# Kernel tuning notes

Measured on AMD Instinct MI355X. Metric: run time of the kernel, lower is better.

Reference implementation:

```python
import jax, jax.numpy as jnp
import numpy as np

B, L = 1, 2048
D_MODEL, N_LAYER, D_INNER = 768, 2, 1536
D_STATE, DT_RANK, D_CONV, OUT_DIM = 16, 48, 4, 128


def setup_inputs() -> dict:
    key = jax.random.key(0)
    ks = jax.random.split(key, 10)
    s = 0.02
    p = {}
    p["x"] = jax.random.normal(ks[0], (B, L, D_MODEL), jnp.float32)
    # stacked per-layer parameters, leading dim = N_LAYER
    p["in_proj_w"] = jax.random.normal(ks[1], (N_LAYER, 2 * D_INNER, D_MODEL), jnp.float32) * s
    p["conv_w"] = jax.random.normal(ks[2], (N_LAYER, D_INNER, D_CONV), jnp.float32) * s
    p["conv_b"] = jnp.zeros((N_LAYER, D_INNER), jnp.float32)
    p["x_proj_w"] = jax.random.normal(ks[3], (N_LAYER, DT_RANK + 2 * D_STATE, D_INNER), jnp.float32) * s
    p["dt_proj_w"] = jax.random.normal(ks[4], (N_LAYER, D_INNER, DT_RANK), jnp.float32) * s
    p["dt_proj_b"] = jax.random.normal(ks[5], (N_LAYER, D_INNER), jnp.float32) * s
    A = jnp.tile(jnp.arange(1, D_STATE + 1, dtype=jnp.float32)[None, :], (D_INNER, 1))
    p["A_log"] = jnp.tile(jnp.log(A)[None], (N_LAYER, 1, 1))
    p["D"] = jnp.ones((N_LAYER, D_INNER), jnp.float32)
    p["out_proj_w"] = jax.random.normal(ks[6], (N_LAYER, D_MODEL, D_INNER), jnp.float32) * s
    p["norm_w"] = jnp.ones((N_LAYER, D_MODEL), jnp.float32)
    p["norm_f_w"] = jnp.ones((D_MODEL,), jnp.float32)
    p["head_w"] = jax.random.normal(ks[7], (OUT_DIM, D_MODEL), jnp.float32) * s
    return p


def rmsnorm(x, w, eps=1e-5):
    return x * jax.lax.rsqrt(jnp.mean(x * x, -1, keepdims=True) + eps) * w


def selective_scan(u, delta, A, Bm, Cm, Dv):
    # u, delta: (b,l,d); A: (d,n); Bm, Cm: (b,l,n); Dv: (d,)
    dA = jnp.exp(jnp.einsum('bld,dn->bldn', delta, A))       # discretized A
    dBu = jnp.einsum('bld,bln->bldn', delta * u, Bm)          # discretized B*u

    def step(s, inp):
        dA_t, dBu_t, C_t = inp                               # (b,d,n),(b,d,n),(b,n)
        s = dA_t * s + dBu_t
        y = jnp.einsum('bdn,bn->bd', s, C_t)
        return s, y

    s0 = jnp.zeros((u.shape[0], u.shape[2], A.shape[1]), u.dtype)
    _, ys = jax.lax.scan(step, s0, (dA.transpose(1, 0, 2, 3), dBu.transpose(1, 0, 2, 3), Cm.transpose(1, 0, 2)))
    y = ys.transpose(1, 0, 2)                                # (b,l,d)
    return y + u * Dv


def mamba_block(x, w):
    xr = jnp.einsum('bld,ed->ble', x, w['in_proj_w'])        # (b,l,2*d_inner)
    xin, res = jnp.split(xr, 2, axis=-1)
    # causal depthwise conv1d
    xc = jax.lax.conv_general_dilated(
        xin.transpose(0, 2, 1), w['conv_w'][:, None, :],
        window_strides=(1,), padding=[(D_CONV - 1, 0)],
        dimension_numbers=('NCH', 'OIH', 'NCH'),
        feature_group_count=D_INNER)
    xc = (xc + w['conv_b'][None, :, None]).transpose(0, 2, 1)
    xc = jax.nn.silu(xc)
    # SSM
    A = -jnp.exp(w['A_log'])                                 # (d_inner, d_state)
    proj = jnp.einsum('bld,ed->ble', xc, w['x_proj_w'])
    delta, Bm, Cm = jnp.split(proj, [DT_RANK, DT_RANK + D_STATE], axis=-1)
    delta = jax.nn.softplus(jnp.einsum('blr,dr->bld', delta, w['dt_proj_w']) + w['dt_proj_b'])
    y = selective_scan(xc, delta, A, Bm, Cm, w['D'])
    y = y * jax.nn.silu(res)
    return jnp.einsum('bld,ed->ble', y, w['out_proj_w'])


def reference(x, in_proj_w, conv_w, conv_b, x_proj_w, dt_proj_w, dt_proj_b,
              A_log, D, out_proj_w, norm_w, norm_f_w, head_w):
    stacked = dict(in_proj_w=in_proj_w, conv_w=conv_w, conv_b=conv_b,
                   x_proj_w=x_proj_w, dt_proj_w=dt_proj_w, dt_proj_b=dt_proj_b,
                   A_log=A_log, D=D, out_proj_w=out_proj_w)
    for i in range(N_LAYER):
        w = {k: v[i] for k, v in stacked.items()}
        x = x + mamba_block(rmsnorm(x, norm_w[i]), w)        # pre-norm residual block
    x = rmsnorm(x, norm_f_w)
    return jnp.einsum('bld,od->blo', x, head_w)              # lm_head (no bias)
```

## Files before the change

kernel.cpp:

```cpp
#include <hip/hip_runtime.h>
#include <hip/hip_bf16.h>
#include <stdint.h>

#define LSEQ 2048
#define DM 768
#define DI 1536
#define NCH 128
#define CHK 16

typedef __bf16 bf16;
typedef short short8 __attribute__((ext_vector_type(8)));
typedef float floatx4 __attribute__((ext_vector_type(4)));
typedef bf16 bf16x8 __attribute__((ext_vector_type(8)));

__device__ inline float silu_f(float x){ return x / (1.f + __expf(-x)); }

__device__ __forceinline__ void g2l16(const bf16* g, bf16* l){
  __builtin_amdgcn_global_load_lds(
      (const __attribute__((address_space(1))) void*)g,
      (__attribute__((address_space(3))) void*)l, 16, 0, 0);
}

__device__ inline int bf16_flag(const void* dvv){
  return (*(const unsigned*)dvv == 0x3F803F80u) ? 1 : 0;
}

__device__ inline float ldin(const void* p, long i, int f){
  return f ? (float)((const bf16*)p)[i] : ((const float*)p)[i];
}

__device__ __forceinline__ void ld8(const void* src, long i, int f, float* o){
  if(f){
    bf16x8 v = *(const bf16x8*)((const bf16*)src + i);
    #pragma unroll
    for(int k = 0; k < 8; k++) o[k] = (float)v[k];
  } else {
    float4 a = ((const float4*)src)[i >> 2];
    float4 b = ((const float4*)src)[(i >> 2) + 1];
    o[0]=a.x; o[1]=a.y; o[2]=a.z; o[3]=a.w; o[4]=b.x; o[5]=b.y; o[6]=b.z; o[7]=b.w;
  }
}
__device__ __forceinline__ void st8_bf(bf16* dst, long i, const float* o){
  bf16x8 v;
  #pragma unroll
  for(int k = 0; k < 8; k++) v[k] = (bf16)o[k];
  *(bf16x8*)(dst + i) = v;
}
__device__ __forceinline__ void st8_f32(float* dst, long i, const float* o){
  ((float4*)dst)[i >> 2]       = make_float4(o[0], o[1], o[2], o[3]);
  ((float4*)dst)[(i >> 2) + 1] = make_float4(o[4], o[5], o[6], o[7]);
}

#define NB_INW  2304
#define NB_OUTW 1152
#define NB_HW   48
#define NB_X    768
#define NB_ALOG 24
#define NB_XPW  192
#define NB_DTW  96
#define NB_SM   12
#define NB_TOT  (NB_INW+NB_OUTW+NB_HW+NB_X+NB_ALOG+NB_XPW+NB_DTW+NB_SM)

__global__ __launch_bounds__(256) void k_canon(const void* x_, const void* inw_,
    const void* cw_, const void* cb_, const void* xpw_, const void* dtw_,
    const void* dtb_, const void* dvv_, const void* alog_, const void* outw_,
    const void* nw_, const void* nfw_, const void* hw_,
    float* x0, bf16* inw, float* cw, float* cb, bf16* xpw, bf16* dtw, float* dtb,
    float* alog, float* dv, bf16* outw, float* nw, float* nfw, bf16* hw){
  int f = bf16_flag(dvv_);
  int b = blockIdx.x;
  int t = threadIdx.x;
  float o[8];
  if(b < NB_INW + NB_OUTW + NB_HW){
    const void* src; bf16* dst; long off;
    if(b < NB_INW){ src = inw_; dst = inw; off = (long)b*2048; }
    else if(b < NB_INW + NB_OUTW){ src = outw_; dst = outw; off = (long)(b - NB_INW)*2048; }
    else { src = hw_; dst = hw; off = (long)(b - NB_INW - NB_OUTW)*2048; }
    long i = off + t*8;
    if(f){ *(bf16x8*)(dst + i) = *(const bf16x8*)((const bf16*)src + i); }
    else { ld8(src, i, 0, o); st8_bf(dst, i, o); }
    return;
  }
  b -= NB_INW + NB_OUTW + NB_HW;
  if(b < NB_X + NB_ALOG){
    const void* src; float* dst; long off;
    if(b < NB_X){ src = x_; dst = x0; off = (long)b*2048; }
    else { src = alog_; dst = alog; off = (long)(b - NB_X)*2048; }
    long i = off + t*8;
    ld8(src, i, f, o);
    st8_f32(dst, i, o);
    return;
  }
  b -= NB_X + NB_ALOG;
  if(b < NB_XPW){
    long j = (long)b*2048 + t*8;
    int layer = (int)(j / (128*DI));
    int rem = (int)(j % (128*DI));
    int r = rem / DI, c = rem % DI;
    if(r < 80){
      ld8(xpw_, ((long)layer*80 + r)*DI + c, f, o);
    } else {
      for(int k = 0; k < 8; k++) o[k] = 0.f;
    }
    st8_bf(xpw, j, o);
    return;
  }
  b -= NB_XPW;
  if(b < NB_DTW){
    long j = (long)b*2048 + t*8;
    int layer = (int)(j / (DI*64));
    int rem = (int)(j % (DI*64));
    int r = rem / 64, c = rem % 64;
    if(c < 48){
      ld8(dtw_, ((long)layer*DI + r)*48 + c, f, o);
    } else {
      for(int k = 0; k < 8; k++) o[k] = 0.f;
    }
    st8_bf(dtw, j, o);
    return;
  }
  b -= NB_DTW;
  for(int idx = b*256 + t; idx < 23808; idx += NB_SM*256){
    int j = idx;
    if(j < 12288){ cw[j] = ldin(cw_, j, f); continue; } j -= 12288;
    if(j < 3072){ cb[j] = ldin(cb_, j, f); continue; } j -= 3072;
    if(j < 3072){ dtb[j] = ldin(dtb_, j, f); continue; } j -= 3072;
    if(j < 3072){ dv[j] = ldin(dvv_, j, f); continue; } j -= 3072;
    if(j < 1536){ nw[j] = ldin(nw_, j, f); continue; } j -= 1536;
    nfw[j] = ldin(nfw_, j, f);
  }
}

__global__ __launch_bounds__(256) void k_rmsnorm(const float* __restrict__ x,
    const float* __restrict__ w, bf16* __restrict__ out){
  int row = blockIdx.x;
  const float* xr = x + row*DM;
  int t = threadIdx.x;
  float v0 = xr[t], v1 = xr[t+256], v2 = xr[t+512];
  float ss = v0*v0 + v1*v1 + v2*v2;
  #pragma unroll
  for(int o = 32; o; o >>= 1) ss += __shfl_down(ss, o, 64);
  __shared__ float red[4];
  int lane = t & 63, wid = t >> 6;
  if(lane == 0) red[wid] = ss;
  __syncthreads();
  ss = red[0] + red[1] + red[2] + red[3];
  float rs = rsqrtf(ss / DM + 1e-5f);
  out[row*DM + t]       = (bf16)(v0 * rs * w[t]);
  out[row*DM + t + 256] = (bf16)(v1 * rs * w[t+256]);
  out[row*DM + t + 512] = (bf16)(v2 * rs * w[t+512]);
}

template<int SPLITK, int MODE>
__global__ __launch_bounds__(256) void k_gemm(
    const bf16* __restrict__ A, const bf16* __restrict__ B, void* Cv,
    int K, int ldc, const float* __restrict__ aux){
  __shared__ bf16 sA[64*32];
  __shared__ bf16 sB[128*32];
  int bm0 = blockIdx.y*64, bn0 = blockIdx.x*128;
  int tid = threadIdx.x;
  int lane = tid & 63, wid = tid >> 6;
  int wn = wid*32;
  int quad = lane >> 4, lr = lane & 15;
  const int klen = K / SPLITK;
  const int kbeg = (SPLITK > 1) ? blockIdx.z * klen : 0;
  const bf16* Ag = A + (size_t)(bm0 + (tid>>2))*K + kbeg + (tid&3)*8;
  const bf16* Bg = B + (size_t)(bn0 + (tid>>2))*K + kbeg + (tid&3)*8;
  floatx4 acc[4][2] = {};
  for(int k0 = 0; k0 < klen; k0 += 32){
    __syncthreads();
    g2l16(Ag, sA + tid*8);
    g2l16(Bg, sB + tid*8);
    g2l16(Bg + 64*K, sB + 2048 + tid*8);
    __syncthreads();
    short8 af[4], bf_[2];
    #pragma unroll
    for(int i = 0; i < 4; i++)
      af[i]  = *(const short8*)(sA + (i*16 + lr)*32 + quad*8);
    #pragma unroll
    for(int j = 0; j < 2; j++)
      bf_[j] = *(const short8*)(sB + (wn + j*16 + lr)*32 + quad*8);
    #pragma unroll
    for(int i = 0; i < 4; i++)
      #pragma unroll
      for(int j = 0; j < 2; j++)
        acc[i][j] = __builtin_amdgcn_mfma_f32_16x16x32_bf16(af[i], bf_[j], acc[i][j], 0, 0, 0);
    Ag += 32; Bg += 32;
  }
  float* Cf = (float*)Cv + ((MODE == 5) ? (size_t)blockIdx.z * LSEQ * ldc : 0);
  bf16* Cb = (bf16*)Cv;
  #pragma unroll
  for(int i = 0; i < 4; i++){
    #pragma unroll
    for(int j = 0; j < 2; j++){
      #pragma unroll
      for(int r = 0; r < 4; r++){
        int grow = bm0 + i*16 + quad*4 + r;
        int gcol = bn0 + wn + j*16 + lr;
        float v = acc[i][j][r];
        if(MODE == 0){
          Cb[(size_t)grow*ldc + gcol] = (bf16)v;
        } else if(MODE == 1){
          v += aux[gcol];
          v = fmaxf(v, 0.f) + log1pf(__expf(-fabsf(v)));
          Cb[(size_t)grow*ldc + gcol] = (bf16)v;
        } else {
          Cf[(size_t)grow*ldc + gcol] = v;
        }
      }
    }
  }
  (void)aux;
}

__global__ __launch_bounds__(256) void k_epi_xproj(const float* __restrict__ part,
    float* __restrict__ proj, bf16* __restrict__ dtin){
  int idx = blockIdx.x*256 + threadIdx.x;
  float s = 0.f;
  #pragma unroll
  for(int z = 0; z < 8; z++) s += part[(size_t)z*LSEQ*128 + idx];
  int row = idx >> 7, col = idx & 127;
  if(col < 80) proj[row*80 + col] = s;
  if(col < 64) dtin[row*64 + col] = (col < 48) ? (bf16)s : (bf16)0.f;
}

__global__ __launch_bounds__(256) void k_epi_out_norm(const float* __restrict__ part,
    const float* __restrict__ resid, const float* __restrict__ w,
    float* __restrict__ xws, bf16* __restrict__ xn){
  int row = blockIdx.x;
  int t = threadIdx.x;
  float v[3]; float ss = 0.f;
  #pragma unroll
  for(int k = 0; k < 3; k++){
    long i = (long)row*DM + t + k*256;
    float s = part[i] + part[(long)LSEQ*DM + i] + resid[i];
    xws[i] = s; v[k] = s; ss += s*s;
  }
  #pragma unroll
  for(int o = 32; o; o >>= 1) ss += __shfl_down(ss, o, 64);
  __shared__ float red[4];
  if((t & 63) == 0) red[t >> 6] = ss;
  __syncthreads();
  ss = red[0] + red[1] + red[2] + red[3];
  float rs = rsqrtf(ss / DM + 1e-5f);
  #pragma unroll
  for(int k = 0; k < 3; k++){
    int col = t + k*256;
    xn[(long)row*DM + col] = (bf16)(v[k] * rs * w[col]);
  }
}

__global__ __launch_bounds__(256) void k_epi_head(const float* __restrict__ part,
    const void* dvv, void* out){
  int idx = blockIdx.x*256 + threadIdx.x;
  const int N = LSEQ*128;
  float s = part[idx] + part[N+idx] + part[2*N+idx] + part[3*N+idx];
  if(bf16_flag(dvv)) ((bf16*)out)[idx] = (bf16)s;
  else               ((float*)out)[idx] = s;
}

__global__ __launch_bounds__(256) void k_conv(const bf16* __restrict__ xr,
    const float* __restrict__ cw, const float* __restrict__ cb,
    bf16* __restrict__ xcb){
  int d = blockIdx.x*256 + threadIdx.x;
  int l0 = blockIdx.y*16;
  float w0 = cw[d*4+0], w1 = cw[d*4+1], w2 = cw[d*4+2], w3 = cw[d*4+3];
  float bias = cb[d];
  float xm3 = (l0 >= 3) ? (float)xr[(l0-3)*(2*DI) + d] : 0.f;
  float xm2 = (l0 >= 2) ? (float)xr[(l0-2)*(2*DI) + d] : 0.f;
  float xm1 = (l0 >= 1) ? (float)xr[(l0-1)*(2*DI) + d] : 0.f;
  #pragma unroll
  for(int tl = 0; tl < 16; tl++){
    int l = l0 + tl;
    float xc = (float)xr[l*(2*DI) + d];
    float acc = bias + xm3*w0 + xm2*w1 + xm1*w2 + xc*w3;
    xcb[l*DI + d] = (bf16)silu_f(acc);
    xm3 = xm2; xm2 = xm1; xm1 = xc;
  }
}

__global__ __launch_bounds__(256) void k_scan1(
    const bf16* __restrict__ delta, const bf16* __restrict__ u,
    const float* __restrict__ proj, const float* __restrict__ alog,
    float* __restrict__ Aprod, float* __restrict__ Bsum){
  int d = blockIdx.y*256 + threadIdx.x;
  int c = blockIdx.x;
  __shared__ float Bl[CHK*16];
  {
    int t = threadIdx.x >> 4, n = threadIdx.x & 15;
    Bl[threadIdx.x] = proj[(c*CHK + t)*80 + 48 + n];
  }
  __syncthreads();
  const float L2E = 1.44269504f;
  float An2[16], ap[16], s[16];
  #pragma unroll
  for(int n = 0; n < 16; n++){ An2[n] = -__expf(alog[d*16+n]) * L2E; ap[n] = 1.f; s[n] = 0.f; }
  int t0 = c*CHK;
  float dt = (float)delta[t0*DI + d];
  float uu = (float)u[t0*DI + d];
  #pragma unroll
  for(int tl = 0; tl < CHK; tl++){
    float dtn = 0.f, un = 0.f;
    if(tl + 1 < CHK){
      dtn = (float)delta[(t0+tl+1)*DI + d];
      un = (float)u[(t0+tl+1)*DI + d];
    }
    float du = dt * uu;
    #pragma unroll
    for(int n = 0; n < 16; n++){
      float e = exp2f(dt * An2[n]);
      s[n] = e*s[n] + du*Bl[tl*16+n];
      ap[n] *= e;
    }
    dt = dtn; uu = un;
  }
  int base = (c*DI + d)*16;
  #pragma unroll
  for(int n = 0; n < 16; n++){ Aprod[base+n] = ap[n]; Bsum[base+n] = s[n]; }
}

__global__ __launch_bounds__(256) void k_scan2(float* __restrict__ Aprod,
    const float* __restrict__ Bsum){
  int idx = blockIdx.x*256 + threadIdx.x;
  float s = 0.f;
  for(int c = 0; c < NCH; c++){
    int o = c*DI*16 + idx;
    float a = Aprod[o], b = Bsum[o];
    Aprod[o] = s;
    s = a*s + b;
  }
}

__global__ __launch_bounds__(256) void k_scan3(
    const bf16* __restrict__ delta, const bf16* __restrict__ u,
    const float* __restrict__ proj, const float* __restrict__ alog,
    const float* __restrict__ dvp, const float* __restrict__ Sinit,
    const bf16* __restrict__ xr, bf16* __restrict__ ybar){
  int d = blockIdx.y*256 + threadIdx.x;
  int c = blockIdx.x;
  __shared__ float Bl[CHK*16], Cl[CHK*16];
  {
    int t = threadIdx.x >> 4, n = threadIdx.x & 15;
    Bl[threadIdx.x] = proj[(c*CHK + t)*80 + 48 + n];
    Cl[threadIdx.x] = proj[(c*CHK + t)*80 + 64 + n];
  }
  __syncthreads();
  const float L2E = 1.44269504f;
  float An2[16], s[16];
  #pragma unroll
  for(int n = 0; n < 16; n++) An2[n] = -__expf(alog[d*16+n]) * L2E;
  int base = (c*DI + d)*16;
  #pragma unroll
  for(int n = 0; n < 16; n++) s[n] = Sinit[base+n];
  float Dd = dvp[d];
  int t0 = c*CHK;
  float dt = (float)delta[t0*DI + d];
  float uu = (float)u[t0*DI + d];
  float res = (float)xr[t0*(2*DI) + DI + d];
  #pragma unroll
  for(int tl = 0; tl < CHK; tl++){
    float dtn = 0.f, un = 0.f, rn = 0.f;
    if(tl + 1 < CHK){
      dtn = (float)delta[(t0+tl+1)*DI + d];
      un = (float)u[(t0+tl+1)*DI + d];
      rn = (float)xr[(t0+tl+1)*(2*DI) + DI + d];
    }
    float du = dt * uu;
    float y = 0.f;
    #pragma unroll
    for(int n = 0; n < 16; n++){
      float e = exp2f(dt * An2[n]);
      s[n] = e*s[n] + du*Bl[tl*16+n];
      y += s[n]*Cl[tl*16+n];
    }
    y += uu * Dd;
    ybar[(t0+tl)*DI + d] = (bf16)(y * silu_f(res));
    dt = dtn; uu = un; res = rn;
  }
}

extern "C" void kernel_launch(void* const* d_in, const int* in_sizes, int n_in,
                              void* d_out, int out_size, void* d_ws, size_t ws_size,
                              hipStream_t stream){
  const void* x_   = d_in[0];
  const void* inw_ = d_in[1];
  const void* cw_  = d_in[2];
  const void* cb_  = d_in[3];
  const void* xpw_ = d_in[4];
  const void* dtw_ = d_in[5];
  const void* dtb_ = d_in[6];
  const void* alog_= d_in[7];
  const void* dvv_ = d_in[8];
  const void* outw_= d_in[9];
  const void* nw_  = d_in[10];
  const void* nfw_ = d_in[11];
  const void* hw_  = d_in[12];

  char* p = (char*)d_ws;
  auto alloc = [&](size_t n){ char* r = p; p += (n + 255) & ~(size_t)255; return r; };
  float* x0  = (float*)alloc((size_t)LSEQ*DM*4);
  bf16* inw  = (bf16*)alloc((size_t)2*2*DI*DM*2);
  float* cw  = (float*)alloc((size_t)2*DI*4*4);
  float* cb  = (float*)alloc((size_t)2*DI*4);
  bf16* xpw  = (bf16*)alloc((size_t)2*128*DI*2);
  bf16* dtw  = (bf16*)alloc((size_t)2*DI*64*2);
  float* dtb = (float*)alloc((size_t)2*DI*4);
  float* alog= (float*)alloc((size_t)2*DI*16*4);
  float* dv  = (float*)alloc((size_t)2*DI*4);
  bf16* outw = (bf16*)alloc((size_t)2*DM*DI*2);
  float* nw  = (float*)alloc((size_t)2*DM*4);
  float* nfw = (float*)alloc((size_t)DM*4);
  bf16* hw   = (bf16*)alloc((size_t)128*DM*2);
  bf16* xn   = (bf16*)alloc((size_t)LSEQ*DM*2);
  bf16* xr   = (bf16*)alloc((size_t)LSEQ*2*DI*2);
  bf16* xcb  = (bf16*)alloc((size_t)LSEQ*DI*2);
  float* proj= (float*)alloc((size_t)LSEQ*80*4);
  bf16* dtin = (bf16*)alloc((size_t)LSEQ*64*2);
  bf16* delta= (bf16*)alloc((size_t)LSEQ*DI*2);
  float* Aprod=(float*)alloc((size_t)NCH*DI*16*4);
  float* Bsum =(float*)alloc((size_t)NCH*DI*16*4);
  bf16* ybar = (bf16*)alloc((size_t)LSEQ*DI*2);
  float* xws = (float*)alloc((size_t)LSEQ*DM*4);
  float* part = (float*)alloc((size_t)2*LSEQ*DM*4);

  k_canon<<<NB_TOT, 256, 0, stream>>>(x_, inw_, cw_, cb_, xpw_, dtw_, dtb_, dvv_,
      alog_, outw_, nw_, nfw_, hw_,
      x0, inw, cw, cb, xpw, dtw, dtb, alog, dv, outw, nw, nfw, hw);

  k_rmsnorm<<<LSEQ, 256, 0, stream>>>(x0, nw, xn);
  const float* xcur = x0;
  for(int i = 0; i < 2; i++){
    k_gemm<1,0><<<dim3(2*DI/128, LSEQ/64), 256, 0, stream>>>(
        xn, inw + (size_t)i*2*DI*DM, xr, DM, 2*DI, nullptr);
    k_conv<<<dim3(DI/256, LSEQ/16), 256, 0, stream>>>(xr, cw + i*DI*4, cb + i*DI, xcb);
    k_gemm<8,5><<<dim3(1, LSEQ/64, 8), 256, 0, stream>>>(
        xcb, xpw + (size_t)i*128*DI, part, DI, 128, nullptr);
    k_epi_xproj<<<LSEQ*128/256, 256, 0, stream>>>(part, proj, dtin);
    k_gemm<1,1><<<dim3(DI/128, LSEQ/64), 256, 0, stream>>>(
        dtin, dtw + (size_t)i*DI*64, delta, 64, DI, dtb + i*DI);
    k_scan1<<<dim3(NCH, DI/256), 256, 0, stream>>>(delta, xcb, proj, alog + i*DI*16, Aprod, Bsum);
    k_scan2<<<DI*16/256, 256, 0, stream>>>(Aprod, Bsum);
    k_scan3<<<dim3(NCH, DI/256), 256, 0, stream>>>(delta, xcb, proj, alog + i*DI*16,
        dv + i*DI, Aprod, xr, ybar);
    k_gemm<2,5><<<dim3(DM/128, LSEQ/64, 2), 256, 0, stream>>>(
        ybar, outw + (size_t)i*DM*DI, part, DI, DM, nullptr);
    k_epi_out_norm<<<LSEQ, 256, 0, stream>>>(part, xcur,
        (i == 0) ? (nw + DM) : nfw, xws, xn);
    xcur = xws;
  }
  k_gemm<4,5><<<dim3(1, LSEQ/64, 4), 256, 0, stream>>>(
      xn, hw, part, DM, 128, nullptr);
  k_epi_head<<<LSEQ*128/256, 256, 0, stream>>>(part, dvv_, d_out);

  (void)in_sizes; (void)n_in; (void)out_size; (void)ws_size;
}
```

Measured before the change: 380.8 us.

## Fuse depthwise conv into x_proj GEMM and scans, fold split-K reduce into consumers

The standalone conv kernel and the x_proj epilogue kernel are removed. The causal conv plus SiLU is now computed on the fly while loading the A tile of the x_proj GEMM, and recomputed inside both scan kernels. The split-K partial sums are reduced directly in the dt-projection GEMM prologue and in the scan B/C loads. This cuts two launches and the xcb/proj/dtin intermediate round trips, at the cost of redundant conv recomputation and repeated 8-way partial reductions in several kernels.

```diff
diff --git a/kernel.cpp b/kernel.cpp
--- a/kernel.cpp
+++ b/kernel.cpp
@@ -198,30 +198,167 @@
         int grow = bm0 + i*16 + quad*4 + r;
         int gcol = bn0 + wn + j*16 + lr;
         float v = acc[i][j][r];
-        if(MODE == 0){
-          Cb[(size_t)grow*ldc + gcol] = (bf16)v;
-        } else if(MODE == 1){
-          v += aux[gcol];
-          v = fmaxf(v, 0.f) + log1pf(__expf(-fabsf(v)));
-          Cb[(size_t)grow*ldc + gcol] = (bf16)v;
-        } else {
-          Cf[(size_t)grow*ldc + gcol] = v;
-        }
+        if(MODE == 0) Cb[(size_t)grow*ldc + gcol] = (bf16)v;
+        else          Cf[(size_t)grow*ldc + gcol] = v;
       }
     }
   }
   (void)aux;
 }
 
-__global__ __launch_bounds__(256) void k_epi_xproj(const float* __restrict__ part,
-    float* __restrict__ proj, bf16* __restrict__ dtin){
-  int idx = blockIdx.x*256 + threadIdx.x;
-  float s = 0.f;
-  #pragma unroll
-  for(int z = 0; z < 8; z++) s += part[(size_t)z*LSEQ*128 + idx];
-  int row = idx >> 7, col = idx & 127;
-  if(col < 80) proj[row*80 + col] = s;
-  if(col < 64) dtin[row*64 + col] = (col < 48) ? (bf16)s : (bf16)0.f;
+__global__ __launch_bounds__(256) void k_xproj(
+    const bf16* __restrict__ xr, const bf16* __restrict__ B,
+    const float* __restrict__ cw, const float* __restrict__ cb,
+    float* __restrict__ part){
+  __shared__ bf16 sA[64*32];
+  __shared__ bf16 sB[128*32];
+  int bm0 = blockIdx.y*64;
+  int tid = threadIdx.x;
+  int lane = tid & 63, wid = tid >> 6;
+  int wn = wid*32;
+  int quad = lane >> 4, lr = lane & 15;
+  const int kbeg = blockIdx.z * (DI/8);
+  int r = tid >> 2;
+  int l = bm0 + r;
+  int cs = (tid & 3)*8;
+  const bf16* Bg = B + (size_t)(tid>>2)*DI + kbeg + (tid&3)*8;
+  floatx4 acc[4][2] = {};
+  for(int k0 = 0; k0 < DI/8; k0 += 32){
+    int c = kbeg + k0 + cs;
+    float4 w4[8]; float bias[8];
+    #pragma unroll
+    for(int j = 0; j < 8; j++){ w4[j] = ((const float4*)cw)[c+j]; bias[j] = cb[c+j]; }
+    float xv[4][8];
+    #pragma unroll
+    for(int k = 0; k < 4; k++){
+      int lt = l - 3 + k;
+      if(lt >= 0){
+        bf16x8 v = *(const bf16x8*)(xr + (size_t)lt*(2*DI) + c);
+        #pragma unroll
+        for(int j = 0; j < 8; j++) xv[k][j] = (float)v[j];
+      } else {
+        #pragma unroll
+        for(int j = 0; j < 8; j++) xv[k][j] = 0.f;
+      }
+    }
+    float o[8];
+    #pragma unroll
+    for(int j = 0; j < 8; j++){
+      float a = bias[j] + xv[0][j]*w4[j].x + xv[1][j]*w4[j].y
+                        + xv[2][j]*w4[j].z + xv[3][j]*w4[j].w;
+      o[j] = silu_f(a);
+    }
+    __syncthreads();
+    {
+      bf16x8 v;
+      #pragma unroll
+      for(int j = 0; j < 8; j++) v[j] = (bf16)o[j];
+      *(bf16x8*)(sA + r*32 + cs) = v;
+    }
+    g2l16(Bg, sB + tid*8);
+    g2l16(Bg + 64*DI, sB + 2048 + tid*8);
+    __syncthreads();
+    short8 af[4], bf_[2];
+    #pragma unroll
+    for(int i = 0; i < 4; i++)
+      af[i]  = *(const short8*)(sA + (i*16 + lr)*32 + quad*8);
+    #pragma unroll
+    for(int j = 0; j < 2; j++)
+      bf_[j] = *(const short8*)(sB + (wn + j*16 + lr)*32 + quad*8);
+    #pragma unroll
+    for(int i = 0; i < 4; i++)
+      #pragma unroll
+      for(int j = 0; j < 2; j++)
+        acc[i][j] = __builtin_amdgcn_mfma_f32_16x16x32_bf16(af[i], bf_[j], acc[i][j], 0, 0, 0);
+    Bg += 32;
+  }
+  float* Cf = part + (size_t)blockIdx.z * LSEQ * 128;
+  #pragma unroll
+  for(int i = 0; i < 4; i++){
+    #pragma unroll
+    for(int j = 0; j < 2; j++){
+      #pragma unroll
+      for(int r2 = 0; r2 < 4; r2++){
+        int grow = bm0 + i*16 + quad*4 + r2;
+        int gcol = wn + j*16 + lr;
+        Cf[(size_t)grow*128 + gcol] = acc[i][j][r2];
+      }
+    }
+  }
+}
+
+__global__ __launch_bounds__(256) void k_dtgemm(
+    const float* __restrict__ part, const bf16* __restrict__ dtw,
+    const float* __restrict__ dtb, bf16* __restrict__ delta){
+  __shared__ bf16 sA[64*32];
+  __shared__ bf16 sB[128*32];
+  int bm0 = blockIdx.y*64, bn0 = blockIdx.x*128;
+  int tid = threadIdx.x;
+  int lane = tid & 63, wid = tid >> 6;
+  int wn = wid*32;
+  int quad = lane >> 4, lr = lane & 15;
+  int r = tid >> 2;
+  int l = bm0 + r;
+  int cs = (tid & 3)*8;
+  const bf16* Bg = dtw + (size_t)(bn0 + (tid>>2))*64 + (tid&3)*8;
+  floatx4 acc[4][2] = {};
+  #pragma unroll
+  for(int k0 = 0; k0 < 64; k0 += 32){
+    int c = k0 + cs;
+    float o[8];
+    if(c < 48){
+      #pragma unroll
+      for(int j = 0; j < 8; j++) o[j] = 0.f;
+      #pragma unroll
+      for(int z = 0; z < 8; z++){
+        const float* pr = part + (size_t)z*LSEQ*128 + (size_t)l*128 + c;
+        float4 a = *(const float4*)pr;
+        float4 b = *(const float4*)(pr + 4);
+        o[0]+=a.x; o[1]+=a.y; o[2]+=a.z; o[3]+=a.w;
+        o[4]+=b.x; o[5]+=b.y; o[6]+=b.z; o[7]+=b.w;
+      }
+    } else {
+      #pragma unroll
+      for(int j = 0; j < 8; j++) o[j] = 0.f;
+    }
+    __syncthreads();
+    {
+      bf16x8 v;
+      #pragma unroll
+      for(int j = 0; j < 8; j++) v[j] = (bf16)o[j];
+      *(bf16x8*)(sA + r*32 + cs) = v;
+    }
+    g2l16(Bg, sB + tid*8);
+    g2l16(Bg + 64*64, sB + 2048 + tid*8);
+    __syncthreads();
+    short8 af[4], bf_[2];
+    #pragma unroll
+    for(int i = 0; i < 4; i++)
+      af[i]  = *(const short8*)(sA + (i*16 + lr)*32 + quad*8);
+    #pragma unroll
+    for(int j = 0; j < 2; j++)
+      bf_[j] = *(const short8*)(sB + (wn + j*16 + lr)*32 + quad*8);
+    #pragma unroll
+    for(int i = 0; i < 4; i++)
+      #pragma unroll
+      for(int j = 0; j < 2; j++)
+        acc[i][j] = __builtin_amdgcn_mfma_f32_16x16x32_bf16(af[i], bf_[j], acc[i][j], 0, 0, 0);
+    Bg += 32;
+  }
+  #pragma unroll
+  for(int i = 0; i < 4; i++){
+    #pragma unroll
+    for(int j = 0; j < 2; j++){
+      #pragma unroll
+      for(int r2 = 0; r2 < 4; r2++){
+        int grow = bm0 + i*16 + quad*4 + r2;
+        int gcol = bn0 + wn + j*16 + lr;
+        float v = acc[i][j][r2] + dtb[gcol];
+        v = fmaxf(v, 0.f) + log1pf(__expf(-fabsf(v)));
+        delta[(size_t)grow*DI + gcol] = (bf16)v;
+      }
+    }
+  }
 }
 
 __global__ __launch_bounds__(256) void k_epi_out_norm(const float* __restrict__ part,
@@ -259,52 +396,40 @@
   else               ((float*)out)[idx] = s;
 }
 
-__global__ __launch_bounds__(256) void k_conv(const bf16* __restrict__ xr,
-    const float* __restrict__ cw, const float* __restrict__ cb,
-    bf16* __restrict__ xcb){
-  int d = blockIdx.x*256 + threadIdx.x;
-  int l0 = blockIdx.y*16;
-  float w0 = cw[d*4+0], w1 = cw[d*4+1], w2 = cw[d*4+2], w3 = cw[d*4+3];
-  float bias = cb[d];
-  float xm3 = (l0 >= 3) ? (float)xr[(l0-3)*(2*DI) + d] : 0.f;
-  float xm2 = (l0 >= 2) ? (float)xr[(l0-2)*(2*DI) + d] : 0.f;
-  float xm1 = (l0 >= 1) ? (float)xr[(l0-1)*(2*DI) + d] : 0.f;
-  #pragma unroll
-  for(int tl = 0; tl < 16; tl++){
-    int l = l0 + tl;
-    float xc = (float)xr[l*(2*DI) + d];
-    float acc = bias + xm3*w0 + xm2*w1 + xm1*w2 + xc*w3;
-    xcb[l*DI + d] = (bf16)silu_f(acc);
-    xm3 = xm2; xm2 = xm1; xm1 = xc;
-  }
-}
-
 __global__ __launch_bounds__(256) void k_scan1(
-    const bf16* __restrict__ delta, const bf16* __restrict__ u,
-    const float* __restrict__ proj, const float* __restrict__ alog,
+    const bf16* __restrict__ delta, const bf16* __restrict__ xr,
+    const float* __restrict__ part, const float* __restrict__ cw,
+    const float* __restrict__ cb, const float* __restrict__ alog,
     float* __restrict__ Aprod, float* __restrict__ Bsum){
   int d = blockIdx.y*256 + threadIdx.x;
   int c = blockIdx.x;
   __shared__ float Bl[CHK*16];
   {
     int t = threadIdx.x >> 4, n = threadIdx.x & 15;
-    Bl[threadIdx.x] = proj[(c*CHK + t)*80 + 48 + n];
+    float s = 0.f;
+    #pragma unroll
+    for(int z = 0; z < 8; z++)
+      s += part[(size_t)z*LSEQ*128 + (size_t)(c*CHK + t)*128 + 48 + n];
+    Bl[threadIdx.x] = s;
   }
   __syncthreads();
   const float L2E = 1.44269504f;
   float An2[16], ap[16], s[16];
   #pragma unroll
   for(int n = 0; n < 16; n++){ An2[n] = -__expf(alog[d*16+n]) * L2E; ap[n] = 1.f; s[n] = 0.f; }
+  float4 w4 = ((const float4*)cw)[d];
+  float bias = cb[d];
   int t0 = c*CHK;
-  float dt = (float)delta[t0*DI + d];
-  float uu = (float)u[t0*DI + d];
+  float xm3 = (t0 >= 3) ? (float)xr[(size_t)(t0-3)*(2*DI) + d] : 0.f;
+  float xm2 = (t0 >= 2) ? (float)xr[(size_t)(t0-2)*(2*DI) + d] : 0.f;
+  float xm1 = (t0 >= 1) ? (float)xr[(size_t)(t0-1)*(2*DI) + d] : 0.f;
+  float dt = (float)delta[(size_t)t0*DI + d];
   #pragma unroll
   for(int tl = 0; tl < CHK; tl++){
-    float dtn = 0.f, un = 0.f;
-    if(tl + 1 < CHK){
-      dtn = (float)delta[(t0+tl+1)*DI + d];
-      un = (float)u[(t0+tl+1)*DI + d];
-    }
+    float dtn = (tl + 1 < CHK) ? (float)delta[(size_t)(t0+tl+1)*DI + d] : 0.f;
+    float xc = (float)xr[(size_t)(t0+tl)*(2*DI) + d];
+    float uu = silu_f(bias + xm3*w4.x + xm2*w4.y + xm1*w4.z + xc*w4.w);
+    xm3 = xm2; xm2 = xm1; xm1 = xc;
     float du = dt * uu;
     #pragma unroll
     for(int n = 0; n < 16; n++){
@@ -312,7 +437,7 @@
       s[n] = e*s[n] + du*Bl[tl*16+n];
       ap[n] *= e;
     }
-    dt = dtn; uu = un;
+    dt = dtn;
   }
   int base = (c*DI + d)*16;
   #pragma unroll
@@ -332,17 +457,25 @@
 }
 
 __global__ __launch_bounds__(256) void k_scan3(
-    const bf16* __restrict__ delta, const bf16* __restrict__ u,
-    const float* __restrict__ proj, const float* __restrict__ alog,
+    const bf16* __restrict__ delta, const bf16* __restrict__ xr,
+    const float* __restrict__ part, const float* __restrict__ cw,
+    const float* __restrict__ cb, const float* __restrict__ alog,
     const float* __restrict__ dvp, const float* __restrict__ Sinit,
-    const bf16* __restrict__ xr, bf16* __restrict__ ybar){
+    bf16* __restrict__ ybar){
   int d = blockIdx.y*256 + threadIdx.x;
   int c = blockIdx.x;
   __shared__ float Bl[CHK*16], Cl[CHK*16];
   {
     int t = threadIdx.x >> 4, n = threadIdx.x & 15;
-    Bl[threadIdx.x] = proj[(c*CHK + t)*80 + 48 + n];
-    Cl[threadIdx.x] = proj[(c*CHK + t)*80 + 64 + n];
+    float sb = 0.f, sc = 0.f;
+    #pragma unroll
+    for(int z = 0; z < 8; z++){
+      const float* pr = part + (size_t)z*LSEQ*128 + (size_t)(c*CHK + t)*128;
+      sb += pr[48 + n];
+      sc += pr[64 + n];
+    }
+    Bl[threadIdx.x] = sb;
+    Cl[threadIdx.x] = sc;
   }
   __syncthreads();
   const float L2E = 1.44269504f;
@@ -353,18 +486,24 @@
   #pragma unroll
   for(int n = 0; n < 16; n++) s[n] = Sinit[base+n];
   float Dd = dvp[d];
+  float4 w4 = ((const float4*)cw)[d];
+  float bias = cb[d];
   int t0 = c*CHK;
-  float dt = (float)delta[t0*DI + d];
-  float uu = (float)u[t0*DI + d];
-  float res = (float)xr[t0*(2*DI) + DI + d];
+  float xm3 = (t0 >= 3) ? (float)xr[(size_t)(t0-3)*(2*DI) + d] : 0.f;
+  float xm2 = (t0 >= 2) ? (float)xr[(size_t)(t0-2)*(2*DI) + d] : 0.f;
+  float xm1 = (t0 >= 1) ? (float)xr[(size_t)(t0-1)*(2*DI) + d] : 0.f;
+  float dt = (float)delta[(size_t)t0*DI + d];
+  float res = (float)xr[(size_t)t0*(2*DI) + DI + d];
   #pragma unroll
   for(int tl = 0; tl < CHK; tl++){
-    float dtn = 0.f, un = 0.f, rn = 0.f;
+    float dtn = 0.f, rn = 0.f;
     if(tl + 1 < CHK){
-      dtn = (float)delta[(t0+tl+1)*DI + d];
-      un = (float)u[(t0+tl+1)*DI + d];
-      rn = (float)xr[(t0+tl+1)*(2*DI) + DI + d];
-    }
+      dtn = (float)delta[(size_t)(t0+tl+1)*DI + d];
+      rn = (float)xr[(size_t)(t0+tl+1)*(2*DI) + DI + d];
+    }
+    float xc = (float)xr[(size_t)(t0+tl)*(2*DI) + d];
+    float uu = silu_f(bias + xm3*w4.x + xm2*w4.y + xm1*w4.z + xc*w4.w);
+    xm3 = xm2; xm2 = xm1; xm1 = xc;
     float du = dt * uu;
     float y = 0.f;
     #pragma unroll
@@ -374,8 +513,8 @@
       y += s[n]*Cl[tl*16+n];
     }
     y += uu * Dd;
-    ybar[(t0+tl)*DI + d] = (bf16)(y * silu_f(res));
-    dt = dtn; uu = un; res = rn;
+    ybar[(size_t)(t0+tl)*DI + d] = (bf16)(y * silu_f(res));
+    dt = dtn; res = rn;
   }
 }
 
@@ -413,9 +552,6 @@
   bf16* hw   = (bf16*)alloc((size_t)128*DM*2);
   bf16* xn   = (bf16*)alloc((size_t)LSEQ*DM*2);
   bf16* xr   = (bf16*)alloc((size_t)LSEQ*2*DI*2);
-  bf16* xcb  = (bf16*)alloc((size_t)LSEQ*DI*2);
-  float* proj= (float*)alloc((size_t)LSEQ*80*4);
-  bf16* dtin = (bf16*)alloc((size_t)LSEQ*64*2);
   bf16* delta= (bf16*)alloc((size_t)LSEQ*DI*2);
   float* Aprod=(float*)alloc((size_t)NCH*DI*16*4);
   float* Bsum =(float*)alloc((size_t)NCH*DI*16*4);
@@ -432,16 +568,15 @@
   for(int i = 0; i < 2; i++){
     k_gemm<1,0><<<dim3(2*DI/128, LSEQ/64), 256, 0, stream>>>(
         xn, inw + (size_t)i*2*DI*DM, xr, DM, 2*DI, nullptr);
-    k_conv<<<dim3(DI/256, LSEQ/16), 256, 0, stream>>>(xr, cw + i*DI*4, cb + i*DI, xcb);
-    k_gemm<8,5><<<dim3(1, LSEQ/64, 8), 256, 0, stream>>>(
-        xcb, xpw + (size_t)i*128*DI, part, DI, 128, nullptr);
-    k_epi_xproj<<<LSEQ*128/256, 256, 0, stream>>>(part, proj, dtin);
-    k_gemm<1,1><<<dim3(DI/128, LSEQ/64), 256, 0, stream>>>(
-        dtin, dtw + (size_t)i*DI*64, delta, 64, DI, dtb + i*DI);
-    k_scan1<<<dim3(NCH, DI/256), 256, 0, stream>>>(delta, xcb, proj, alog + i*DI*16, Aprod, Bsum);
+    k_xproj<<<dim3(1, LSEQ/64, 8), 256, 0, stream>>>(
+        xr, xpw + (size_t)i*128*DI, cw + i*DI*4, cb + i*DI, part);
+    k_dtgemm<<<dim3(DI/128, LSEQ/64), 256, 0, stream>>>(
+        part, dtw + (size_t)i*DI*64, dtb + i*DI, delta);
+    k_scan1<<<dim3(NCH, DI/256), 256, 0, stream>>>(delta, xr, part,
+        cw + i*DI*4, cb + i*DI, alog + i*DI*16, Aprod, Bsum);
     k_scan2<<<DI*16/256, 256, 0, stream>>>(Aprod, Bsum);
-    k_scan3<<<dim3(NCH, DI/256), 256, 0, stream>>>(delta, xcb, proj, alog + i*DI*16,
-        dv + i*DI, Aprod, xr, ybar);
+    k_scan3<<<dim3(NCH, DI/256), 256, 0, stream>>>(delta, xr, part,
+        cw + i*DI*4, cb + i*DI, alog + i*DI*16, dv + i*DI, Aprod, ybar);
     k_gemm<2,5><<<dim3(DM/128, LSEQ/64, 2), 256, 0, stream>>>(
         ybar, outw + (size_t)i*DM*DI, part, DI, DM, nullptr);
     k_epi_out_norm<<<LSEQ, 256, 0, stream>>>(part, xcur,
```

Measured after the change: 418.2 us. 9.8% more time.
